# Performance work log

Hardware: AMD Instinct MI355X
Metric: run time of the kernel (lower is better)

The kernel has to match this reference:

```python
import jax, jax.numpy as jnp
import numpy as np

N = 32768      # num nodes
F = 128        # raw node feature dim
D = 128        # embedding_dim
E = 524288     # num edges (avg degree 16)
L = 8          # transformer depth
H = 8          # heads
CS = 32        # target_cluster_size
NC = 10        # num classes
K = N // CS    # num clusters (all full -> pad branch is a no-op)


def _leaky_relu(x):
    return jnp.where(x >= 0, x, 0.2 * x)


def _gat(h_in, src, dst, W, a_src, a_dst, b):
    # PyG GATConv, heads=1, with self-loops already appended to src/dst
    h = h_in @ W                                             # [N, D]
    e = _leaky_relu((h @ a_src)[src] + (h @ a_dst)[dst])     # [E+N]
    m = jax.ops.segment_max(e, dst, num_segments=N)
    ex = jnp.exp(e - m[dst])
    denom = jax.ops.segment_sum(ex, dst, num_segments=N)
    alpha = ex / denom[dst]
    return jax.ops.segment_sum(h[src] * alpha[:, None], dst, num_segments=N) + b


def _ln(x, s, b):
    m = x.mean(-1, keepdims=True)
    v = ((x - m) ** 2).mean(-1, keepdims=True)
    return (x - m) * jax.lax.rsqrt(v + 1e-5) * s + b


def setup_inputs() -> dict:
    key = jax.random.key(0)
    ks = jax.random.split(key, 20)
    rn = lambda k, s, sc=0.05: jax.random.normal(k, s, jnp.float32) * sc
    return dict(
        x=jax.random.normal(ks[0], (N, F), jnp.float32),
        edge_index=jax.random.randint(ks[1], (2, E), 0, N),
        node_order=jax.random.permutation(ks[2], N).astype(jnp.int32),
        W_in=rn(ks[3], (F, D)), b_in=jnp.zeros(D, jnp.float32),
        Wg1=rn(ks[4], (D, D)), as1=rn(ks[5], (D,)), ad1=rn(ks[6], (D,)), bg1=jnp.zeros(D, jnp.float32),
        Wg2=rn(ks[7], (D, D)), as2=rn(ks[8], (D,)), ad2=rn(ks[9], (D,)), bg2=jnp.zeros(D, jnp.float32),
        W_emb=rn(ks[10], (CS * D, D), 0.02), b_emb=jnp.zeros(D, jnp.float32),
        cls_tok=rn(ks[11], (D,)),
        ln1_s=jnp.ones((L, D), jnp.float32), ln1_b=jnp.zeros((L, D), jnp.float32),
        Wqkv=rn(ks[12], (L, D, 3 * D)), bqkv=jnp.zeros((L, 3 * D), jnp.float32),
        Wo=rn(ks[13], (L, D, D)), bo=jnp.zeros((L, D), jnp.float32),
        ln2_s=jnp.ones((L, D), jnp.float32), ln2_b=jnp.zeros((L, D), jnp.float32),
        Wf1=rn(ks[14], (L, D, 4 * D)), bf1=jnp.zeros((L, 4 * D), jnp.float32),
        Wf2=rn(ks[15], (L, 4 * D, D)), bf2=jnp.zeros((L, D), jnp.float32),
        Wc=rn(ks[16], (D, NC)), bc=jnp.zeros(NC, jnp.float32),
    )


def reference(x, edge_index, node_order, W_in, b_in, Wg1, as1, ad1, bg1,
              Wg2, as2, ad2, bg2, W_emb, b_emb, cls_tok,
              ln1_s, ln1_b, Wqkv, bqkv, Wo, bo, ln2_s, ln2_b,
              Wf1, bf1, Wf2, bf2, Wc, bc):
    loops = jnp.arange(N, dtype=edge_index.dtype)
    src = jnp.concatenate([edge_index[0], loops])
    dst = jnp.concatenate([edge_index[1], loops])
    h = x @ W_in + b_in
    h = _gat(h, src, dst, Wg1, as1, ad1, bg1)
    h = _gat(h, src, dst, Wg2, as2, ad2, bg2)
    # irregular cluster gather, then per-cluster linear embedding (32*D -> D)
    flat = h[node_order].reshape(K, CS * D)
    emb = flat @ W_emb + b_emb                               # [K, D]
    t = jnp.concatenate([cls_tok[None, :], emb], axis=0)     # [K+1, D]
    dh = D // H
    scale = dh ** -0.5
    for l in range(L):                                       # pre-norm transformer
        u = _ln(t, ln1_s[l], ln1_b[l])
        qkv = u @ Wqkv[l] + bqkv[l]
        q, k, v = [a.reshape(-1, H, dh) for a in jnp.split(qkv, 3, axis=-1)]
        att = jax.nn.softmax(jnp.einsum('qhd,khd->hqk', q, k) * scale, axis=-1)
        o = jnp.einsum('hqk,khd->qhd', att, v).reshape(-1, D) @ Wo[l] + bo[l]
        t = t + o
        u = _ln(t, ln2_s[l], ln2_b[l])
        t = t + jax.nn.gelu(u @ Wf1[l] + bf1[l]) @ Wf2[l] + bf2[l]
    return (t[0] @ Wc + bc)[None, :]                         # [1, NC]
```

## Files before the change

### kernel.cpp

```cpp
#include <hip/hip_runtime.h>
#include <hip/hip_bf16.h>
#include <math.h>

#define NN 32768
#define NE 524288
#define EN_TOT (NE + NN)
#define LL 8
#define SS 1025
#define SPLIT 16

__global__ void hist_kernel(const int* __restrict__ ei, int* __restrict__ cnt) {
    int i = blockIdx.x * 256 + threadIdx.x;
    if (i >= EN_TOT) return;
    int d = (i < NE) ? ei[NE + i] : (i - NE);
    atomicAdd(&cnt[d], 1);
}

__global__ void scan_kernel(const int* __restrict__ cnt, int* __restrict__ offs) {
    __shared__ int wsum[16];
    int t = threadIdx.x;
    int base = t * 32;
    int s = 0;
    #pragma unroll
    for (int j = 0; j < 32; ++j) s += cnt[base + j];
    int lane = t & 63, w = t >> 6;
    int v = s;
    #pragma unroll
    for (int d = 1; d < 64; d <<= 1) {
        int u = __shfl_up(v, d);
        if (lane >= d) v += u;
    }
    if (lane == 63) wsum[w] = v;
    __syncthreads();
    if (t == 0) {
        int a = 0;
        #pragma unroll
        for (int i = 0; i < 16; ++i) { int x = wsum[i]; wsum[i] = a; a += x; }
    }
    __syncthreads();
    int run = wsum[w] + (v - s);
    #pragma unroll
    for (int j = 0; j < 32; ++j) { offs[base + j] = run; run += cnt[base + j]; }
    if (t == 1023) offs[NN] = run;
}

__global__ void scatter_kernel(const int* __restrict__ ei, const int* __restrict__ offs,
                               int* __restrict__ fill, int* __restrict__ csr) {
    int i = blockIdx.x * 256 + threadIdx.x;
    if (i >= EN_TOT) return;
    int s, d;
    if (i < NE) { s = ei[i]; d = ei[NE + i]; } else { s = d = i - NE; }
    int pos = offs[d] + atomicAdd(&fill[d], 1);
    csr[pos] = s;
}

__device__ __forceinline__ float gelu_f(float x) {
    float x3 = x * x * x;
    return 0.5f * x * (1.f + tanhf(0.7978845608028654f * (x + 0.044715f * x3)));
}

__global__ void gemm_f32(const float* __restrict__ A, const float* __restrict__ B,
                         const float* __restrict__ bias, const float* res,
                         float* C, __hip_bfloat16* Cb,
                         const float* __restrict__ asv, const float* __restrict__ adv,
                         float* ssv, float* sdv,
                         int M, int Nn, int K) {
    __shared__ float As[32][66];
    __shared__ float Bs[32][72];
    int t = threadIdx.x;
    int bx = blockIdx.x, by = blockIdx.y;
    int tx = t & 15, ty = t >> 4;
    float acc[4][4] = {};
    int m0 = t >> 3;
    int kk4 = (t & 7) * 4;
    int kb0 = t >> 4;
    int n40 = (t & 15) * 4;

    for (int k0 = 0; k0 < K; k0 += 32) {
        __syncthreads();
        #pragma unroll
        for (int half = 0; half < 2; ++half) {
            int m = m0 + half * 32;
            int row = by * 64 + m;
            float4 v = {0.f, 0.f, 0.f, 0.f};
            if (row < M) v = *(const float4*)&A[(size_t)row * K + k0 + kk4];
            As[kk4 + 0][m] = v.x; As[kk4 + 1][m] = v.y;
            As[kk4 + 2][m] = v.z; As[kk4 + 3][m] = v.w;
        }
        #pragma unroll
        for (int half = 0; half < 2; ++half) {
            int kk = kb0 + half * 16;
            *(float4*)&Bs[kk][n40] = *(const float4*)&B[(size_t)(k0 + kk) * Nn + bx * 64 + n40];
        }
        __syncthreads();
        #pragma unroll
        for (int kk = 0; kk < 32; ++kk) {
            float a0 = As[kk][ty * 4 + 0];
            float a1 = As[kk][ty * 4 + 1];
            float a2 = As[kk][ty * 4 + 2];
            float a3 = As[kk][ty * 4 + 3];
            float4 b4 = *(float4*)&Bs[kk][tx * 4];
            acc[0][0] += a0 * b4.x; acc[0][1] += a0 * b4.y; acc[0][2] += a0 * b4.z; acc[0][3] += a0 * b4.w;
            acc[1][0] += a1 * b4.x; acc[1][1] += a1 * b4.y; acc[1][2] += a1 * b4.z; acc[1][3] += a1 * b4.w;
            acc[2][0] += a2 * b4.x; acc[2][1] += a2 * b4.y; acc[2][2] += a2 * b4.z; acc[2][3] += a2 * b4.w;
            acc[3][0] += a3 * b4.x; acc[3][1] += a3 * b4.y; acc[3][2] += a3 * b4.z; acc[3][3] += a3 * b4.w;
        }
    }
    #pragma unroll
    for (int i = 0; i < 4; ++i) {
        int row = by * 64 + ty * 4 + i;
        if (row < M) {
            #pragma unroll
            for (int j = 0; j < 4; ++j) {
                int col = bx * 64 + tx * 4 + j;
                float v = acc[i][j];
                if (bias) v += bias[col];
                if (res) v += res[(size_t)row * Nn + col];
                acc[i][j] = v;
                C[(size_t)row * Nn + col] = v;
                if (Cb) Cb[(size_t)row * Nn + col] = __float2bfloat16(v);
            }
        }
    }
    if (asv) {
        #pragma unroll
        for (int i = 0; i < 4; ++i) {
            int row = by * 64 + ty * 4 + i;
            float vs = 0.f, vd = 0.f;
            #pragma unroll
            for (int j = 0; j < 4; ++j) {
                int col = bx * 64 + tx * 4 + j;
                vs += acc[i][j] * asv[col];
                vd += acc[i][j] * adv[col];
            }
            #pragma unroll
            for (int m = 8; m >= 1; m >>= 1) { vs += __shfl_xor(vs, m); vd += __shfl_xor(vd, m); }
            if (tx == 0 && row < M) {
                atomicAdd(&ssv[row], vs);
                atomicAdd(&sdv[row], vd);
            }
        }
    }
}

__global__ void bcomb_kernel(const float* __restrict__ b_in, const float* __restrict__ Wg1,
                             float* __restrict__ bcomb) {
    int n = threadIdx.x;
    float s = 0.f;
    for (int k = 0; k < 128; ++k) s += b_in[k] * Wg1[k * 128 + n];
    bcomb[n] = s;
}

__global__ void emb_gemm(const float* __restrict__ h, const float* __restrict__ W,
                         const int* __restrict__ no, float* __restrict__ pbuf) {
    __shared__ float As[32][66];
    __shared__ float Bs[32][72];
    int t = threadIdx.x;
    int bx = blockIdx.x, by = blockIdx.y, sp = blockIdx.z;
    int tx = t & 15, ty = t >> 4;
    float acc[4][4] = {};
    int m0 = t >> 3;
    int kk4 = (t & 7) * 4;
    int kb0 = t >> 4;
    int n40 = (t & 15) * 4;
    int kbase = sp * 256;

    for (int k0 = 0; k0 < 256; k0 += 32) {
        __syncthreads();
        #pragma unroll
        for (int half = 0; half < 2; ++half) {
            int m = m0 + half * 32;
            int row = by * 64 + m;
            int kg = kbase + k0 + kk4;
            int node = no[row * 32 + (kg >> 7)];
            float4 v = *(const float4*)&h[(size_t)node * 128 + (kg & 127)];
            As[kk4 + 0][m] = v.x; As[kk4 + 1][m] = v.y;
            As[kk4 + 2][m] = v.z; As[kk4 + 3][m] = v.w;
        }
        #pragma unroll
        for (int half = 0; half < 2; ++half) {
            int kk = kb0 + half * 16;
            *(float4*)&Bs[kk][n40] = *(const float4*)&W[(size_t)(kbase + k0 + kk) * 128 + bx * 64 + n40];
        }
        __syncthreads();
        #pragma unroll
        for (int kk = 0; kk < 32; ++kk) {
            float a0 = As[kk][ty * 4 + 0];
            float a1 = As[kk][ty * 4 + 1];
            float a2 = As[kk][ty * 4 + 2];
            float a3 = As[kk][ty * 4 + 3];
            float4 b4 = *(float4*)&Bs[kk][tx * 4];
            acc[0][0] += a0 * b4.x; acc[0][1] += a0 * b4.y; acc[0][2] += a0 * b4.z; acc[0][3] += a0 * b4.w;
            acc[1][0] += a1 * b4.x; acc[1][1] += a1 * b4.y; acc[1][2] += a1 * b4.z; acc[1][3] += a1 * b4.w;
            acc[2][0] += a2 * b4.x; acc[2][1] += a2 * b4.y; acc[2][2] += a2 * b4.z; acc[2][3] += a2 * b4.w;
            acc[3][0] += a3 * b4.x; acc[3][1] += a3 * b4.y; acc[3][2] += a3 * b4.z; acc[3][3] += a3 * b4.w;
        }
    }
    float* C = pbuf + (size_t)sp * (1024 * 128);
    #pragma unroll
    for (int i = 0; i < 4; ++i) {
        int row = by * 64 + ty * 4 + i;
        #pragma unroll
        for (int j = 0; j < 4; ++j)
            C[(size_t)row * 128 + bx * 64 + tx * 4 + j] = acc[i][j];
    }
}

__global__ void emb_reduce(const float* __restrict__ pbuf, const float* __restrict__ b_emb,
                           float* __restrict__ out) {
    int i = blockIdx.x * 256 + threadIdx.x;
    float s = b_emb[i & 127];
    #pragma unroll
    for (int sp = 0; sp < SPLIT; ++sp) s += pbuf[(size_t)sp * 131072 + i];
    out[i] = s;
}

__global__ void gat_aggregate(const unsigned* __restrict__ hWb, const int* __restrict__ offs,
                              const int* __restrict__ csr, const float* __restrict__ ssrc,
                              const float* __restrict__ sdst, const float* __restrict__ bias,
                              float* __restrict__ out) {
    int lane = threadIdx.x & 63;
    int n = blockIdx.x * 4 + (threadIdx.x >> 6);
    int beg = offs[n], end = offs[n + 1];
    float sd = sdst[n];
    float mymax = -INFINITY;
    for (int p = beg + lane; p < end; p += 64) {
        float e = ssrc[csr[p]] + sd;
        e = (e >= 0.f) ? e : 0.2f * e;
        mymax = fmaxf(mymax, e);
    }
    #pragma unroll
    for (int m = 32; m >= 1; m >>= 1) mymax = fmaxf(mymax, __shfl_xor(mymax, m));
    float mysum = 0.f;
    for (int p = beg + lane; p < end; p += 64) {
        float e = ssrc[csr[p]] + sd;
        e = (e >= 0.f) ? e : 0.2f * e;
        mysum += __expf(e - mymax);
    }
    #pragma unroll
    for (int m = 32; m >= 1; m >>= 1) mysum += __shfl_xor(mysum, m);
    float inv = 1.f / mysum;
    float acc0 = 0.f, acc1 = 0.f;
    for (int p = beg; p < end; ++p) {
        int s = csr[p];
        float e = ssrc[s] + sd;
        e = (e >= 0.f) ? e : 0.2f * e;
        float al = __expf(e - mymax) * inv;
        unsigned u = hWb[(size_t)s * 64 + lane];
        float f0 = __uint_as_float(u << 16);
        float f1 = __uint_as_float(u & 0xffff0000u);
        acc0 += al * f0;
        acc1 += al * f1;
    }
    float2 ov;
    ov.x = acc0 + bias[2 * lane];
    ov.y = acc1 + bias[2 * lane + 1];
    *(float2*)&out[(size_t)n * 128 + 2 * lane] = ov;
}

__global__ __launch_bounds__(256) void qkv_slice(
        const float* __restrict__ tb, const float* __restrict__ s1, const float* __restrict__ b1,
        const float* __restrict__ Wq, const float* __restrict__ bq, float* __restrict__ qkv) {
    __shared__ float u[4][128];
    __shared__ float red[4][2][128];
    __shared__ float ws[8192];
    int t = threadIdx.x;
    int r0 = blockIdx.x * 4, sl = blockIdx.y;
    int col = t & 127, kh = t >> 7;
    {
        int rw = t >> 6, lane = t & 63;
        int row = r0 + rw;
        float a0 = 0.f, a1 = 0.f;
        if (row < SS) {
            a0 = tb[(size_t)row * 128 + lane];
            a1 = tb[(size_t)row * 128 + 64 + lane];
        }
        float sm = a0 + a1;
        #pragma unroll
        for (int m = 32; m >= 1; m >>= 1) sm += __shfl_xor(sm, m);
        float mean = sm * (1.f / 128.f);
        float d0 = a0 - mean, d1 = a1 - mean;
        float vv = d0 * d0 + d1 * d1;
        #pragma unroll
        for (int m = 32; m >= 1; m >>= 1) vv += __shfl_xor(vv, m);
        float rs = rsqrtf(vv * (1.f / 128.f) + 1e-5f);
        u[rw][lane] = d0 * rs * s1[lane] + b1[lane];
        u[rw][64 + lane] = d1 * rs * s1[64 + lane] + b1[64 + lane];
    }
    float acc[4] = {};
    for (int k0 = 0; k0 < 128; k0 += 64) {
        __syncthreads();
        const float* src = Wq + (size_t)k0 * 384 + sl * 128;
        #pragma unroll
        for (int i = 0; i < 8; ++i) {
            int idx = i * 256 + t;
            int kk = idx >> 5, c4 = (idx & 31) * 4;
            ((float4*)ws)[idx] = *(const float4*)&src[(size_t)kk * 384 + c4];
        }
        __syncthreads();
        int kb = kh * 32;
        #pragma unroll
        for (int kq = 0; kq < 32; kq += 4) {
            float a4[4][4];
            #pragma unroll
            for (int i = 0; i < 4; ++i)
                *(float4*)a4[i] = *(const float4*)&u[i][k0 + kb + kq];
            #pragma unroll
            for (int q = 0; q < 4; ++q) {
                float b = ws[(kb + kq + q) * 128 + col];
                #pragma unroll
                for (int i = 0; i < 4; ++i) acc[i] += a4[i][q] * b;
            }
        }
    }
    __syncthreads();
    #pragma unroll
    for (int i = 0; i < 4; ++i) red[i][kh][col] = acc[i];
    __syncthreads();
    if (t < 128) {
        float bqv = bq[sl * 128 + t];
        #pragma unroll
        for (int i = 0; i < 4; ++i) {
            int row = r0 + i;
            if (row < SS)
                qkv[(size_t)row * 384 + sl * 128 + t] = red[i][0][t] + red[i][1][t] + bqv;
        }
    }
}

__global__ __launch_bounds__(256) void proj_ln2(
        const float* __restrict__ ao, const float* __restrict__ Wo, const float* __restrict__ bo,
        const float* __restrict__ s2, const float* __restrict__ b2, const float* __restrict__ bf2,
        float* __restrict__ tb, float* __restrict__ ub) {
    __shared__ float bufA[4][128];
    __shared__ float tn[4][128];
    __shared__ float red[4][2][128];
    __shared__ float ws[8192];
    int t = threadIdx.x;
    int r0 = blockIdx.x * 4;
    int lane = t & 63;
    int col = t & 127, kh = t >> 7;
    {
        int rw = t >> 6;
        int row = r0 + rw;
        float a0 = 0.f, a1 = 0.f;
        if (row < SS) {
            a0 = ao[(size_t)row * 128 + lane];
            a1 = ao[(size_t)row * 128 + 64 + lane];
        }
        bufA[rw][lane] = a0;
        bufA[rw][64 + lane] = a1;
    }
    float pp[4] = {};
    for (int k0 = 0; k0 < 128; k0 += 64) {
        __syncthreads();
        const float4* src = (const float4*)&Wo[(size_t)k0 * 128];
        #pragma unroll
        for (int i = 0; i < 8; ++i) ((float4*)ws)[i * 256 + t] = src[i * 256 + t];
        __syncthreads();
        int kb = kh * 32;
        #pragma unroll
        for (int kq = 0; kq < 32; kq += 4) {
            float a4[4][4];
            #pragma unroll
            for (int i = 0; i < 4; ++i)
                *(float4*)a4[i] = *(const float4*)&bufA[i][k0 + kb + kq];
            #pragma unroll
            for (int q = 0; q < 4; ++q) {
                float b = ws[(kb + kq + q) * 128 + col];
                #pragma unroll
                for (int i = 0; i < 4; ++i) pp[i] += a4[i][q] * b;
            }
        }
    }
    __syncthreads();
    #pragma unroll
    for (int i = 0; i < 4; ++i) red[i][kh][col] = pp[i];
    __syncthreads();
    if (t < 128) {
        #pragma unroll
        for (int i = 0; i < 4; ++i) {
            int row = r0 + i;
            float v = 0.f;
            if (row < SS) {
                v = red[i][0][t] + red[i][1][t] + bo[t] + tb[(size_t)row * 128 + t];
                tb[(size_t)row * 128 + t] = v + bf2[t];
            }
            tn[i][t] = v;
        }
    }
    __syncthreads();
    {
        int rw = t >> 6;
        int row = r0 + rw;
        float a0 = tn[rw][lane], a1 = tn[rw][64 + lane];
        float sm = a0 + a1;
        #pragma unroll
        for (int m = 32; m >= 1; m >>= 1) sm += __shfl_xor(sm, m);
        float mean = sm * (1.f / 128.f);
        float d0 = a0 - mean, d1 = a1 - mean;
        float vv = d0 * d0 + d1 * d1;
        #pragma unroll
        for (int m = 32; m >= 1; m >>= 1) vv += __shfl_xor(vv, m);
        float rs = rsqrtf(vv * (1.f / 128.f) + 1e-5f);
        if (row < SS) {
            ub[(size_t)row * 128 + lane] = d0 * rs * s2[lane] + b2[lane];
            ub[(size_t)row * 128 + 64 + lane] = d1 * rs * s2[64 + lane] + b2[64 + lane];
        }
    }
}

__global__ __launch_bounds__(256) void ffn_part(
        const float* __restrict__ ub, const float* __restrict__ Wf1, const float* __restrict__ bf1,
        const float* __restrict__ Wf2, float* __restrict__ tb) {
    __shared__ float u[4][128];
    __shared__ float g[4][128];
    __shared__ float red[4][2][128];
    __shared__ float ws[8192];
    int t = threadIdx.x;
    int r0 = blockIdx.x * 4, sl = blockIdx.y;
    int col = t & 127, kh = t >> 7;
    {
        int rw = t >> 6, lane = t & 63;
        int row = r0 + rw;
        float a0 = 0.f, a1 = 0.f;
        if (row < SS) {
            a0 = ub[(size_t)row * 128 + lane];
            a1 = ub[(size_t)row * 128 + 64 + lane];
        }
        u[rw][lane] = a0;
        u[rw][64 + lane] = a1;
    }
    float a1c[4] = {};
    for (int k0 = 0; k0 < 128; k0 += 64) {
        __syncthreads();
        const float* src = Wf1 + (size_t)k0 * 512 + sl * 128;
        #pragma unroll
        for (int i = 0; i < 8; ++i) {
            int idx = i * 256 + t;
            int kk = idx >> 5, c4 = (idx & 31) * 4;
            ((float4*)ws)[idx] = *(const float4*)&src[(size_t)kk * 512 + c4];
        }
        __syncthreads();
        int kb = kh * 32;
        #pragma unroll
        for (int kq = 0; kq < 32; kq += 4) {
            float a4[4][4];
            #pragma unroll
            for (int i = 0; i < 4; ++i)
                *(float4*)a4[i] = *(const float4*)&u[i][k0 + kb + kq];
            #pragma unroll
            for (int q = 0; q < 4; ++q) {
                float b = ws[(kb + kq + q) * 128 + col];
                #pragma unroll
                for (int i = 0; i < 4; ++i) a1c[i] += a4[i][q] * b;
            }
        }
    }
    __syncthreads();
    #pragma unroll
    for (int i = 0; i < 4; ++i) red[i][kh][col] = a1c[i];
    __syncthreads();
    if (t < 128) {
        float bv = bf1[sl * 128 + t];
        #pragma unroll
        for (int i = 0; i < 4; ++i)
            g[i][t] = gelu_f(red[i][0][t] + red[i][1][t] + bv);
    }
    float a2c[4] = {};
    for (int k0 = 0; k0 < 128; k0 += 64) {
        __syncthreads();
        const float4* src = (const float4*)&Wf2[(size_t)(sl * 128 + k0) * 128];
        #pragma unroll
        for (int i = 0; i < 8; ++i) ((float4*)ws)[i * 256 + t] = src[i * 256 + t];
        __syncthreads();
        int kb = kh * 32;
        #pragma unroll
        for (int kq = 0; kq < 32; kq += 4) {
            float a4[4][4];
            #pragma unroll
            for (int i = 0; i < 4; ++i)
                *(float4*)a4[i] = *(const float4*)&g[i][k0 + kb + kq];
            #pragma unroll
            for (int q = 0; q < 4; ++q) {
                float b = ws[(kb + kq + q) * 128 + col];
                #pragma unroll
                for (int i = 0; i < 4; ++i) a2c[i] += a4[i][q] * b;
            }
        }
    }
    __syncthreads();
    #pragma unroll
    for (int i = 0; i < 4; ++i) red[i][kh][col] = a2c[i];
    __syncthreads();
    if (t < 128) {
        #pragma unroll
        for (int i = 0; i < 4; ++i) {
            int row = r0 + i;
            if (row < SS)
                atomicAdd(&tb[(size_t)row * 128 + t], red[i][0][t] + red[i][1][t]);
        }
    }
}

__global__ void attn_kernel(const float* __restrict__ qkv, float* __restrict__ ao) {
    __shared__ float Kl[64][20];
    __shared__ float Vl[64][20];
    int h = blockIdx.y;
    int t = threadIdx.x;
    int sub = t & 15;
    int qr = blockIdx.x * 16 + (t >> 4);
    bool active = qr < SS;
    float q[16];
    if (active) {
        #pragma unroll
        for (int d = 0; d < 16; ++d) q[d] = qkv[(size_t)qr * 384 + h * 16 + d];
    }
    float m = -INFINITY, sum = 0.f;
    float acc[16] = {};
    for (int j0 = 0; j0 < SS; j0 += 64) {
        __syncthreads();
        int j = t >> 2, dg = (t & 3) * 4;
        if (j0 + j < SS) {
            const float* row = qkv + (size_t)(j0 + j) * 384 + h * 16 + dg;
            *(float4*)&Kl[j][dg] = *(const float4*)(row + 128);
            *(float4*)&Vl[j][dg] = *(const float4*)(row + 256);
        }
        __syncthreads();
        if (active) {
            int jmax = min(64, SS - j0);
            for (int jj = sub; jj < jmax; jj += 16) {
                float4 ka = *(const float4*)&Kl[jj][0];
                float4 kb = *(const float4*)&Kl[jj][4];
                float4 kc = *(const float4*)&Kl[jj][8];
                float4 kd = *(const float4*)&Kl[jj][12];
                float sc = q[0]*ka.x + q[1]*ka.y + q[2]*ka.z + q[3]*ka.w
                         + q[4]*kb.x + q[5]*kb.y + q[6]*kb.z + q[7]*kb.w
                         + q[8]*kc.x + q[9]*kc.y + q[10]*kc.z + q[11]*kc.w
                         + q[12]*kd.x + q[13]*kd.y + q[14]*kd.z + q[15]*kd.w;
                sc *= 0.25f;
                float4 va = *(const float4*)&Vl[jj][0];
                float4 vb = *(const float4*)&Vl[jj][4];
                float4 vc = *(const float4*)&Vl[jj][8];
                float4 vd = *(const float4*)&Vl[jj][12];
                float vv[16] = {va.x, va.y, va.z, va.w, vb.x, vb.y, vb.z, vb.w,
                                vc.x, vc.y, vc.z, vc.w, vd.x, vd.y, vd.z, vd.w};
                if (sc <= m) {
                    float p = __expf(sc - m);
                    sum += p;
                    #pragma unroll
                    for (int d = 0; d < 16; ++d) acc[d] += p * vv[d];
                } else {
                    float c = __expf(m - sc);
                    sum = sum * c + 1.f;
                    #pragma unroll
                    for (int d = 0; d < 16; ++d) acc[d] = acc[d] * c + vv[d];
                    m = sc;
                }
            }
        }
    }
    if (active) {
        #pragma unroll
        for (int msk = 1; msk < 16; msk <<= 1) {
            float mo = __shfl_xor(m, msk);
            float so = __shfl_xor(sum, msk);
            float vo[16];
            #pragma unroll
            for (int d = 0; d < 16; ++d) vo[d] = __shfl_xor(acc[d], msk);
            float mn = fmaxf(m, mo);
            float c1 = __expf(m - mn), c2 = __expf(mo - mn);
            sum = sum * c1 + so * c2;
            #pragma unroll
            for (int d = 0; d < 16; ++d) acc[d] = acc[d] * c1 + vo[d] * c2;
            m = mn;
        }
        if (sub == 0) {
            float inv = 1.f / sum;
            #pragma unroll
            for (int d = 0; d < 16; ++d) ao[(size_t)qr * 128 + h * 16 + d] = acc[d] * inv;
        }
    }
}

__global__ void cls_copy(const float* __restrict__ c, float* __restrict__ t) {
    t[threadIdx.x] = c[threadIdx.x];
}

__global__ void classifier_kernel(const float* __restrict__ t, const float* __restrict__ Wc,
                                  const float* __restrict__ bc, float* __restrict__ out) {
    int j = threadIdx.x;
    if (j < 10) {
        float a = bc[j];
        #pragma unroll
        for (int k = 0; k < 128; ++k) a += t[k] * Wc[k * 10 + j];
        out[j] = a;
    }
}

extern "C" void kernel_launch(void* const* d_in, const int* in_sizes, int n_in,
                              void* d_out, int out_size, void* d_ws, size_t ws_size,
                              hipStream_t stream) {
    (void)in_sizes; (void)n_in; (void)out_size; (void)ws_size;
    const float* x     = (const float*)d_in[0];
    const int*   ei    = (const int*)d_in[1];
    const int*   nord  = (const int*)d_in[2];
    const float* W_in  = (const float*)d_in[3];
    const float* b_in  = (const float*)d_in[4];
    const float* Wg1   = (const float*)d_in[5];
    const float* as1   = (const float*)d_in[6];
    const float* ad1   = (const float*)d_in[7];
    const float* bg1   = (const float*)d_in[8];
    const float* Wg2   = (const float*)d_in[9];
    const float* as2   = (const float*)d_in[10];
    const float* ad2   = (const float*)d_in[11];
    const float* bg2   = (const float*)d_in[12];
    const float* W_emb = (const float*)d_in[13];
    const float* b_emb = (const float*)d_in[14];
    const float* clst  = (const float*)d_in[15];
    const float* ln1s  = (const float*)d_in[16];
    const float* ln1b  = (const float*)d_in[17];
    const float* Wqkv  = (const float*)d_in[18];
    const float* bqkv  = (const float*)d_in[19];
    const float* Wo    = (const float*)d_in[20];
    const float* bo    = (const float*)d_in[21];
    const float* ln2s  = (const float*)d_in[22];
    const float* ln2b  = (const float*)d_in[23];
    const float* Wf1   = (const float*)d_in[24];
    const float* bf1   = (const float*)d_in[25];
    const float* Wf2   = (const float*)d_in[26];
    const float* bf2   = (const float*)d_in[27];
    const float* Wc    = (const float*)d_in[28];
    const float* bc    = (const float*)d_in[29];

    char* w = (char*)d_ws;
    size_t o = 0;
    auto ALLOC = [&](size_t nbytes) -> char* {
        char* p = w + o;
        o += (nbytes + 255) & ~(size_t)255;
        return p;
    };
    int*   cnt   = (int*)ALLOC((size_t)NN * 4);
    int*   fill  = (int*)ALLOC((size_t)NN * 4);
    int*   offs  = (int*)ALLOC((size_t)(NN + 1) * 4);
    int*   csr   = (int*)ALLOC((size_t)EN_TOT * 4);
    float* hA    = (float*)ALLOC((size_t)NN * 128 * 4);
    float* hW    = (float*)ALLOC((size_t)NN * 128 * 4);
    float* h1    = (float*)ALLOC((size_t)NN * 128 * 4);
    __hip_bfloat16* hWb = (__hip_bfloat16*)ALLOC((size_t)NN * 128 * 2);
    float* ssrc  = (float*)ALLOC((size_t)NN * 4);
    float* sdst  = (float*)ALLOC((size_t)NN * 4);
    float* tbuf  = (float*)ALLOC((size_t)SS * 128 * 4);
    float* ubuf  = (float*)ALLOC((size_t)SS * 128 * 4);
    float* qkvb  = (float*)ALLOC((size_t)SS * 384 * 4);
    float* aob   = (float*)ALLOC((size_t)SS * 128 * 4);
    float* Wcomb = (float*)ALLOC((size_t)128 * 128 * 4);
    float* bcomb = (float*)ALLOC((size_t)128 * 4);
    float* pbuf  = hW;

    dim3 blk(256);
    int egrid = (EN_TOT + 255) / 256;

    hipMemsetAsync(cnt, 0, (size_t)NN * 8, stream);
    hist_kernel<<<egrid, blk, 0, stream>>>(ei, cnt);
    scan_kernel<<<1, 1024, 0, stream>>>(cnt, offs);
    scatter_kernel<<<egrid, blk, 0, stream>>>(ei, offs, fill, csr);

    gemm_f32<<<dim3(2, 2), blk, 0, stream>>>(W_in, Wg1, nullptr, nullptr, Wcomb,
                                             nullptr, nullptr, nullptr, nullptr, nullptr,
                                             128, 128, 128);
    bcomb_kernel<<<1, 128, 0, stream>>>(b_in, Wg1, bcomb);

    hipMemsetAsync(ssrc, 0, (size_t)NN * 8, stream);
    gemm_f32<<<dim3(2, 512), blk, 0, stream>>>(x, Wcomb, bcomb, nullptr, hW,
                                               hWb, as1, ad1, ssrc, sdst,
                                               NN, 128, 128);
    gat_aggregate<<<8192, blk, 0, stream>>>((const unsigned*)hWb, offs, csr, ssrc, sdst, bg1, h1);
    hipMemsetAsync(ssrc, 0, (size_t)NN * 8, stream);
    gemm_f32<<<dim3(2, 512), blk, 0, stream>>>(h1, Wg2, nullptr, nullptr, hW,
                                               hWb, as2, ad2, ssrc, sdst,
                                               NN, 128, 128);
    gat_aggregate<<<8192, blk, 0, stream>>>((const unsigned*)hWb, offs, csr, ssrc, sdst, bg2, hA);

    cls_copy<<<1, 128, 0, stream>>>(clst, tbuf);
    emb_gemm<<<dim3(2, 16, SPLIT), blk, 0, stream>>>(hA, W_emb, nord, pbuf);
    emb_reduce<<<512, blk, 0, stream>>>(pbuf, b_emb, tbuf + 128);

    for (int l = 0; l < LL; ++l) {
        qkv_slice<<<dim3(257, 3), blk, 0, stream>>>(tbuf, ln1s + l * 128, ln1b + l * 128,
                                                    Wqkv + (size_t)l * 128 * 384, bqkv + l * 384, qkvb);
        attn_kernel<<<dim3(65, 8), blk, 0, stream>>>(qkvb, aob);
        proj_ln2<<<257, blk, 0, stream>>>(aob, Wo + (size_t)l * 128 * 128, bo + l * 128,
                                          ln2s + l * 128, ln2b + l * 128, bf2 + l * 128,
                                          tbuf, ubuf);
        ffn_part<<<dim3(257, 4), blk, 0, stream>>>(ubuf, Wf1 + (size_t)l * 128 * 512, bf1 + l * 512,
                                                   Wf2 + (size_t)l * 512 * 128, tbuf);
    }
    classifier_kernel<<<1, 64, 0, stream>>>(tbuf, Wc, bc, (float*)d_out);
}
```

Baseline: 874.2 us.

## Split GAT dots out, gather fp32 rows, pre-gather cluster input, deterministic FFN partials

The GEMM epilogue no longer computes the attention logit dots with atomics or emits a bf16 copy. A separate dots kernel computes them per node, and aggregation now reads fp32 features with lane-parallel edge loading and shuffle broadcast. The cluster gather is materialized into a flat buffer before the embedding GEMM. FFN slices write per-slice partial buffers that are summed on read, replacing atomics, and the attention K/V tile grows to 128. This trades extra launches and doubled gather bandwidth (fp32 instead of bf16) for fewer atomics and more memory-level parallelism in the edge loop.

```diff
diff --git a/kernel.cpp b/kernel.cpp
--- a/kernel.cpp
+++ b/kernel.cpp
@@ -8,6 +8,7 @@
 #define LL 8
 #define SS 1025
 #define SPLIT 16
+#define SS128 (SS * 128)
 
 __global__ void hist_kernel(const int* __restrict__ ei, int* __restrict__ cnt) {
     int i = blockIdx.x * 256 + threadIdx.x;
@@ -61,10 +62,7 @@
 
 __global__ void gemm_f32(const float* __restrict__ A, const float* __restrict__ B,
                          const float* __restrict__ bias, const float* res,
-                         float* C, __hip_bfloat16* Cb,
-                         const float* __restrict__ asv, const float* __restrict__ adv,
-                         float* ssv, float* sdv,
-                         int M, int Nn, int K) {
+                         float* C, int M, int Nn, int K) {
     __shared__ float As[32][66];
     __shared__ float Bs[32][72];
     int t = threadIdx.x;
@@ -116,28 +114,7 @@
                 float v = acc[i][j];
                 if (bias) v += bias[col];
                 if (res) v += res[(size_t)row * Nn + col];
-                acc[i][j] = v;
                 C[(size_t)row * Nn + col] = v;
-                if (Cb) Cb[(size_t)row * Nn + col] = __float2bfloat16(v);
-            }
-        }
-    }
-    if (asv) {
-        #pragma unroll
-        for (int i = 0; i < 4; ++i) {
-            int row = by * 64 + ty * 4 + i;
-            float vs = 0.f, vd = 0.f;
-            #pragma unroll
-            for (int j = 0; j < 4; ++j) {
-                int col = bx * 64 + tx * 4 + j;
-                vs += acc[i][j] * asv[col];
-                vd += acc[i][j] * adv[col];
-            }
-            #pragma unroll
-            for (int m = 8; m >= 1; m >>= 1) { vs += __shfl_xor(vs, m); vd += __shfl_xor(vd, m); }
-            if (tx == 0 && row < M) {
-                atomicAdd(&ssv[row], vs);
-                atomicAdd(&sdv[row], vd);
             }
         }
     }
@@ -151,71 +128,21 @@
     bcomb[n] = s;
 }
 
-__global__ void emb_gemm(const float* __restrict__ h, const float* __restrict__ W,
-                         const int* __restrict__ no, float* __restrict__ pbuf) {
-    __shared__ float As[32][66];
-    __shared__ float Bs[32][72];
-    int t = threadIdx.x;
-    int bx = blockIdx.x, by = blockIdx.y, sp = blockIdx.z;
-    int tx = t & 15, ty = t >> 4;
-    float acc[4][4] = {};
-    int m0 = t >> 3;
-    int kk4 = (t & 7) * 4;
-    int kb0 = t >> 4;
-    int n40 = (t & 15) * 4;
-    int kbase = sp * 256;
-
-    for (int k0 = 0; k0 < 256; k0 += 32) {
-        __syncthreads();
-        #pragma unroll
-        for (int half = 0; half < 2; ++half) {
-            int m = m0 + half * 32;
-            int row = by * 64 + m;
-            int kg = kbase + k0 + kk4;
-            int node = no[row * 32 + (kg >> 7)];
-            float4 v = *(const float4*)&h[(size_t)node * 128 + (kg & 127)];
-            As[kk4 + 0][m] = v.x; As[kk4 + 1][m] = v.y;
-            As[kk4 + 2][m] = v.z; As[kk4 + 3][m] = v.w;
-        }
-        #pragma unroll
-        for (int half = 0; half < 2; ++half) {
-            int kk = kb0 + half * 16;
-            *(float4*)&Bs[kk][n40] = *(const float4*)&W[(size_t)(kbase + k0 + kk) * 128 + bx * 64 + n40];
-        }
-        __syncthreads();
-        #pragma unroll
-        for (int kk = 0; kk < 32; ++kk) {
-            float a0 = As[kk][ty * 4 + 0];
-            float a1 = As[kk][ty * 4 + 1];
-            float a2 = As[kk][ty * 4 + 2];
-            float a3 = As[kk][ty * 4 + 3];
-            float4 b4 = *(float4*)&Bs[kk][tx * 4];
-            acc[0][0] += a0 * b4.x; acc[0][1] += a0 * b4.y; acc[0][2] += a0 * b4.z; acc[0][3] += a0 * b4.w;
-            acc[1][0] += a1 * b4.x; acc[1][1] += a1 * b4.y; acc[1][2] += a1 * b4.z; acc[1][3] += a1 * b4.w;
-            acc[2][0] += a2 * b4.x; acc[2][1] += a2 * b4.y; acc[2][2] += a2 * b4.z; acc[2][3] += a2 * b4.w;
-            acc[3][0] += a3 * b4.x; acc[3][1] += a3 * b4.y; acc[3][2] += a3 * b4.z; acc[3][3] += a3 * b4.w;
-        }
-    }
-    float* C = pbuf + (size_t)sp * (1024 * 128);
-    #pragma unroll
-    for (int i = 0; i < 4; ++i) {
-        int row = by * 64 + ty * 4 + i;
-        #pragma unroll
-        for (int j = 0; j < 4; ++j)
-            C[(size_t)row * 128 + bx * 64 + tx * 4 + j] = acc[i][j];
-    }
-}
-
-__global__ void emb_reduce(const float* __restrict__ pbuf, const float* __restrict__ b_emb,
-                           float* __restrict__ out) {
-    int i = blockIdx.x * 256 + threadIdx.x;
-    float s = b_emb[i & 127];
-    #pragma unroll
-    for (int sp = 0; sp < SPLIT; ++sp) s += pbuf[(size_t)sp * 131072 + i];
-    out[i] = s;
-}
-
-__global__ void gat_aggregate(const unsigned* __restrict__ hWb, const int* __restrict__ offs,
+__global__ void dots_kernel(const float* __restrict__ hW, const float* __restrict__ asrc,
+                            const float* __restrict__ adst, float* __restrict__ ss,
+                            float* __restrict__ sd) {
+    int lane = threadIdx.x & 63;
+    int n = blockIdx.x * 4 + (threadIdx.x >> 6);
+    float h0 = hW[(size_t)n * 128 + lane];
+    float h1 = hW[(size_t)n * 128 + 64 + lane];
+    float vs = h0 * asrc[lane] + h1 * asrc[64 + lane];
+    float vd = h0 * adst[lane] + h1 * adst[64 + lane];
+    #pragma unroll
+    for (int m = 32; m >= 1; m >>= 1) { vs += __shfl_xor(vs, m); vd += __shfl_xor(vd, m); }
+    if (lane == 0) { ss[n] = vs; sd[n] = vd; }
+}
+
+__global__ void gat_aggregate(const float* __restrict__ hW, const int* __restrict__ offs,
                               const int* __restrict__ csr, const float* __restrict__ ssrc,
                               const float* __restrict__ sdst, const float* __restrict__ bias,
                               float* __restrict__ out) {
@@ -240,26 +167,124 @@
     #pragma unroll
     for (int m = 32; m >= 1; m >>= 1) mysum += __shfl_xor(mysum, m);
     float inv = 1.f / mysum;
-    float acc0 = 0.f, acc1 = 0.f;
-    for (int p = beg; p < end; ++p) {
-        int s = csr[p];
-        float e = ssrc[s] + sd;
-        e = (e >= 0.f) ? e : 0.2f * e;
-        float al = __expf(e - mymax) * inv;
-        unsigned u = hWb[(size_t)s * 64 + lane];
-        float f0 = __uint_as_float(u << 16);
-        float f1 = __uint_as_float(u & 0xffff0000u);
-        acc0 += al * f0;
-        acc1 += al * f1;
+    float accx = 0.f, accy = 0.f;
+    int deg = end - beg;
+    for (int c0 = 0; c0 < deg; c0 += 64) {
+        int s = 0; float al = 0.f;
+        if (c0 + lane < deg) {
+            s = csr[beg + c0 + lane];
+            float e = ssrc[s] + sd;
+            e = (e >= 0.f) ? e : 0.2f * e;
+            al = __expf(e - mymax) * inv;
+        }
+        int cend = min(64, deg - c0);
+        int p = 0;
+        for (; p + 4 <= cend; p += 4) {
+            int s0 = __shfl(s, p);     float a0 = __shfl(al, p);
+            int s1 = __shfl(s, p + 1); float a1 = __shfl(al, p + 1);
+            int s2 = __shfl(s, p + 2); float a2 = __shfl(al, p + 2);
+            int s3 = __shfl(s, p + 3); float a3 = __shfl(al, p + 3);
+            float2 v0 = *(const float2*)&hW[(size_t)s0 * 128 + lane * 2];
+            float2 v1 = *(const float2*)&hW[(size_t)s1 * 128 + lane * 2];
+            float2 v2 = *(const float2*)&hW[(size_t)s2 * 128 + lane * 2];
+            float2 v3 = *(const float2*)&hW[(size_t)s3 * 128 + lane * 2];
+            accx += a0 * v0.x; accy += a0 * v0.y;
+            accx += a1 * v1.x; accy += a1 * v1.y;
+            accx += a2 * v2.x; accy += a2 * v2.y;
+            accx += a3 * v3.x; accy += a3 * v3.y;
+        }
+        for (; p < cend; ++p) {
+            int sj = __shfl(s, p);
+            float aj = __shfl(al, p);
+            float2 v = *(const float2*)&hW[(size_t)sj * 128 + lane * 2];
+            accx += aj * v.x; accy += aj * v.y;
+        }
     }
     float2 ov;
-    ov.x = acc0 + bias[2 * lane];
-    ov.y = acc1 + bias[2 * lane + 1];
+    ov.x = accx + bias[2 * lane];
+    ov.y = accy + bias[2 * lane + 1];
     *(float2*)&out[(size_t)n * 128 + 2 * lane] = ov;
 }
 
+__global__ void gather_copy(const float* __restrict__ hA, const int* __restrict__ no,
+                            float* __restrict__ flat) {
+    int i = blockIdx.x * 256 + threadIdx.x;
+    int m = i >> 12, j = i & 4095;
+    int node = no[(m << 5) + (j >> 7)];
+    flat[i] = hA[(size_t)node * 128 + (j & 127)];
+}
+
+__global__ void emb_gemm(const float* __restrict__ flat, const float* __restrict__ W,
+                         float* __restrict__ pbuf) {
+    __shared__ float As[32][66];
+    __shared__ float Bs[32][72];
+    int t = threadIdx.x;
+    int bx = blockIdx.x, by = blockIdx.y, sp = blockIdx.z;
+    int tx = t & 15, ty = t >> 4;
+    float acc[4][4] = {};
+    int m0 = t >> 3;
+    int kk4 = (t & 7) * 4;
+    int kb0 = t >> 4;
+    int n40 = (t & 15) * 4;
+    int kbase = sp * 256;
+
+    for (int k0 = 0; k0 < 256; k0 += 32) {
+        __syncthreads();
+        #pragma unroll
+        for (int half = 0; half < 2; ++half) {
+            int m = m0 + half * 32;
+            int row = by * 64 + m;
+            float4 v = *(const float4*)&flat[(size_t)row * 4096 + kbase + k0 + kk4];
+            As[kk4 + 0][m] = v.x; As[kk4 + 1][m] = v.y;
+            As[kk4 + 2][m] = v.z; As[kk4 + 3][m] = v.w;
+        }
+        #pragma unroll
+        for (int half = 0; half < 2; ++half) {
+            int kk = kb0 + half * 16;
+            *(float4*)&Bs[kk][n40] = *(const float4*)&W[(size_t)(kbase + k0 + kk) * 128 + bx * 64 + n40];
+        }
+        __syncthreads();
+        #pragma unroll
+        for (int kk = 0; kk < 32; ++kk) {
+            float a0 = As[kk][ty * 4 + 0];
+            float a1 = As[kk][ty * 4 + 1];
+            float a2 = As[kk][ty * 4 + 2];
+            float a3 = As[kk][ty * 4 + 3];
+            float4 b4 = *(float4*)&Bs[kk][tx * 4];
+            acc[0][0] += a0 * b4.x; acc[0][1] += a0 * b4.y; acc[0][2] += a0 * b4.z; acc[0][3] += a0 * b4.w;
+            acc[1][0] += a1 * b4.x; acc[1][1] += a1 * b4.y; acc[1][2] += a1 * b4.z; acc[1][3] += a1 * b4.w;
+            acc[2][0] += a2 * b4.x; acc[2][1] += a2 * b4.y; acc[2][2] += a2 * b4.z; acc[2][3] += a2 * b4.w;
+            acc[3][0] += a3 * b4.x; acc[3][1] += a3 * b4.y; acc[3][2] += a3 * b4.z; acc[3][3] += a3 * b4.w;
+        }
+    }
+    float* C = pbuf + (size_t)sp * (1024 * 128);
+    #pragma unroll
+    for (int i = 0; i < 4; ++i) {
+        int row = by * 64 + ty * 4 + i;
+        #pragma unroll
+        for (int j = 0; j < 4; ++j)
+            C[(size_t)row * 128 + bx * 64 + tx * 4 + j] = acc[i][j];
+    }
+}
+
+__global__ void emb_reduce(const float* __restrict__ pbuf, const float* __restrict__ b_emb,
+                           const float* __restrict__ cls, float* __restrict__ tb) {
+    int i = blockIdx.x * 256 + threadIdx.x;
+    if (blockIdx.x == 0 && threadIdx.x < 128) tb[threadIdx.x] = cls[threadIdx.x];
+    float s = b_emb[i & 127];
+    #pragma unroll
+    for (int sp = 0; sp < SPLIT; ++sp) s += pbuf[(size_t)sp * 131072 + i];
+    tb[128 + i] = s;
+}
+
+__device__ __forceinline__ float tok_read(const float* __restrict__ tb, const float* __restrict__ P,
+                                          size_t ix) {
+    return tb[ix] + P[ix] + P[SS128 + ix] + P[2 * (size_t)SS128 + ix] + P[3 * (size_t)SS128 + ix];
+}
+
 __global__ __launch_bounds__(256) void qkv_slice(
-        const float* __restrict__ tb, const float* __restrict__ s1, const float* __restrict__ b1,
+        const float* __restrict__ tb, const float* __restrict__ P,
+        const float* __restrict__ s1, const float* __restrict__ b1,
         const float* __restrict__ Wq, const float* __restrict__ bq, float* __restrict__ qkv) {
     __shared__ float u[4][128];
     __shared__ float red[4][2][128];
@@ -272,8 +297,9 @@
         int row = r0 + rw;
         float a0 = 0.f, a1 = 0.f;
         if (row < SS) {
-            a0 = tb[(size_t)row * 128 + lane];
-            a1 = tb[(size_t)row * 128 + 64 + lane];
+            size_t ix = (size_t)row * 128 + lane;
+            a0 = tok_read(tb, P, ix);
+            a1 = tok_read(tb, P, ix + 64);
         }
         float sm = a0 + a1;
         #pragma unroll
@@ -329,7 +355,8 @@
 }
 
 __global__ __launch_bounds__(256) void proj_ln2(
-        const float* __restrict__ ao, const float* __restrict__ Wo, const float* __restrict__ bo,
+        const float* __restrict__ ao, const float* __restrict__ P,
+        const float* __restrict__ Wo, const float* __restrict__ bo,
         const float* __restrict__ s2, const float* __restrict__ b2, const float* __restrict__ bf2,
         float* __restrict__ tb, float* __restrict__ ub) {
     __shared__ float bufA[4][128];
@@ -383,8 +410,10 @@
             int row = r0 + i;
             float v = 0.f;
             if (row < SS) {
-                v = red[i][0][t] + red[i][1][t] + bo[t] + tb[(size_t)row * 128 + t];
-                tb[(size_t)row * 128 + t] = v + bf2[t];
+                size_t ix = (size_t)row * 128 + t;
+                float told = tok_read(tb, P, ix);
+                v = red[i][0][t] + red[i][1][t] + bo[t] + told;
+                tb[ix] = v + bf2[t];
             }
             tn[i][t] = v;
         }
@@ -412,7 +441,7 @@
 
 __global__ __launch_bounds__(256) void ffn_part(
         const float* __restrict__ ub, const float* __restrict__ Wf1, const float* __restrict__ bf1,
-        const float* __restrict__ Wf2, float* __restrict__ tb) {
+        const float* __restrict__ Wf2, float* __restrict__ P) {
     __shared__ float u[4][128];
     __shared__ float g[4][128];
     __shared__ float red[4][2][128];
@@ -498,14 +527,14 @@
         for (int i = 0; i < 4; ++i) {
             int row = r0 + i;
             if (row < SS)
-                atomicAdd(&tb[(size_t)row * 128 + t], red[i][0][t] + red[i][1][t]);
+                P[(size_t)sl * SS128 + (size_t)row * 128 + t] = red[i][0][t] + red[i][1][t];
         }
     }
 }
 
 __global__ void attn_kernel(const float* __restrict__ qkv, float* __restrict__ ao) {
-    __shared__ float Kl[64][20];
-    __shared__ float Vl[64][20];
+    __shared__ float Kl[128][20];
+    __shared__ float Vl[128][20];
     int h = blockIdx.y;
     int t = threadIdx.x;
     int sub = t & 15;
@@ -518,17 +547,19 @@
     }
     float m = -INFINITY, sum = 0.f;
     float acc[16] = {};
-    for (int j0 = 0; j0 < SS; j0 += 64) {
-        __syncthreads();
-        int j = t >> 2, dg = (t & 3) * 4;
+    for (int j0 = 0; j0 < SS; j0 += 128) {
+        __syncthreads();
+        int j = t >> 1, dg = (t & 1) * 8;
         if (j0 + j < SS) {
             const float* row = qkv + (size_t)(j0 + j) * 384 + h * 16 + dg;
-            *(float4*)&Kl[j][dg] = *(const float4*)(row + 128);
-            *(float4*)&Vl[j][dg] = *(const float4*)(row + 256);
+            *(float4*)&Kl[j][dg]     = *(const float4*)(row + 128);
+            *(float4*)&Kl[j][dg + 4] = *(const float4*)(row + 132);
+            *(float4*)&Vl[j][dg]     = *(const float4*)(row + 256);
+            *(float4*)&Vl[j][dg + 4] = *(const float4*)(row + 260);
         }
         __syncthreads();
         if (active) {
-            int jmax = min(64, SS - j0);
+            int jmax = min(128, SS - j0);
             for (int jj = sub; jj < jmax; jj += 16) {
                 float4 ka = *(const float4*)&Kl[jj][0];
                 float4 kb = *(const float4*)&Kl[jj][4];
@@ -583,17 +614,14 @@
     }
 }
 
-__global__ void cls_copy(const float* __restrict__ c, float* __restrict__ t) {
-    t[threadIdx.x] = c[threadIdx.x];
-}
-
-__global__ void classifier_kernel(const float* __restrict__ t, const float* __restrict__ Wc,
-                                  const float* __restrict__ bc, float* __restrict__ out) {
+__global__ void classifier_kernel(const float* __restrict__ tb, const float* __restrict__ P,
+                                  const float* __restrict__ Wc, const float* __restrict__ bc,
+                                  float* __restrict__ out) {
     int j = threadIdx.x;
     if (j < 10) {
         float a = bc[j];
         #pragma unroll
-        for (int k = 0; k < 128; ++k) a += t[k] * Wc[k * 10 + j];
+        for (int k = 0; k < 128; ++k) a += tok_read(tb, P, k) * Wc[k * 10 + j];
         out[j] = a;
     }
 }
@@ -647,16 +675,17 @@
     float* hA    = (float*)ALLOC((size_t)NN * 128 * 4);
     float* hW    = (float*)ALLOC((size_t)NN * 128 * 4);
     float* h1    = (float*)ALLOC((size_t)NN * 128 * 4);
-    __hip_bfloat16* hWb = (__hip_bfloat16*)ALLOC((size_t)NN * 128 * 2);
     float* ssrc  = (float*)ALLOC((size_t)NN * 4);
     float* sdst  = (float*)ALLOC((size_t)NN * 4);
-    float* tbuf  = (float*)ALLOC((size_t)SS * 128 * 4);
-    float* ubuf  = (float*)ALLOC((size_t)SS * 128 * 4);
+    float* tbuf  = (float*)ALLOC((size_t)SS128 * 4);
+    float* ubuf  = (float*)ALLOC((size_t)SS128 * 4);
     float* qkvb  = (float*)ALLOC((size_t)SS * 384 * 4);
-    float* aob   = (float*)ALLOC((size_t)SS * 128 * 4);
+    float* aob   = (float*)ALLOC((size_t)SS128 * 4);
+    float* Pbuf  = (float*)ALLOC((size_t)4 * SS128 * 4);
     float* Wcomb = (float*)ALLOC((size_t)128 * 128 * 4);
     float* bcomb = (float*)ALLOC((size_t)128 * 4);
     float* pbuf  = hW;
+    float* flat  = h1;
 
     dim3 blk(256);
     int egrid = (EN_TOT + 255) / 256;
@@ -666,35 +695,31 @@
     scan_kernel<<<1, 1024, 0, stream>>>(cnt, offs);
     scatter_kernel<<<egrid, blk, 0, stream>>>(ei, offs, fill, csr);
 
-    gemm_f32<<<dim3(2, 2), blk, 0, stream>>>(W_in, Wg1, nullptr, nullptr, Wcomb,
-                                             nullptr, nullptr, nullptr, nullptr, nullptr,
-                                             128, 128, 128);
+    gemm_f32<<<dim3(2, 2), blk, 0, stream>>>(W_in, Wg1, nullptr, nullptr, Wcomb, 128, 128, 128);
     bcomb_kernel<<<1, 128, 0, stream>>>(b_in, Wg1, bcomb);
 
-    hipMemsetAsync(ssrc, 0, (size_t)NN * 8, stream);
-    gemm_f32<<<dim3(2, 512), blk, 0, stream>>>(x, Wcomb, bcomb, nullptr, hW,
-                                               hWb, as1, ad1, ssrc, sdst,
-                                               NN, 128, 128);
-    gat_aggregate<<<8192, blk, 0, stream>>>((const unsigned*)hWb, offs, csr, ssrc, sdst, bg1, h1);
-    hipMemsetAsync(ssrc, 0, (size_t)NN * 8, stream);
-    gemm_f32<<<dim3(2, 512), blk, 0, stream>>>(h1, Wg2, nullptr, nullptr, hW,
-                                               hWb, as2, ad2, ssrc, sdst,
-                                               NN, 128, 128);
-    gat_aggregate<<<8192, blk, 0, stream>>>((const unsigned*)hWb, offs, csr, ssrc, sdst, bg2, hA);
-
-    cls_copy<<<1, 128, 0, stream>>>(clst, tbuf);
-    emb_gemm<<<dim3(2, 16, SPLIT), blk, 0, stream>>>(hA, W_emb, nord, pbuf);
-    emb_reduce<<<512, blk, 0, stream>>>(pbuf, b_emb, tbuf + 128);
+    gemm_f32<<<dim3(2, 512), blk, 0, stream>>>(x, Wcomb, bcomb, nullptr, hW, NN, 128, 128);
+    dots_kernel<<<8192, blk, 0, stream>>>(hW, as1, ad1, ssrc, sdst);
+    gat_aggregate<<<8192, blk, 0, stream>>>(hW, offs, csr, ssrc, sdst, bg1, h1);
+    gemm_f32<<<dim3(2, 512), blk, 0, stream>>>(h1, Wg2, nullptr, nullptr, hW, NN, 128, 128);
+    dots_kernel<<<8192, blk, 0, stream>>>(hW, as2, ad2, ssrc, sdst);
+    gat_aggregate<<<8192, blk, 0, stream>>>(hW, offs, csr, ssrc, sdst, bg2, hA);
+
+    gather_copy<<<16384, blk, 0, stream>>>(hA, nord, flat);
+    emb_gemm<<<dim3(2, 16, SPLIT), blk, 0, stream>>>(flat, W_emb, pbuf);
+    emb_reduce<<<512, blk, 0, stream>>>(pbuf, b_emb, clst, tbuf);
+
+    hipMemsetAsync(Pbuf, 0, (size_t)4 * SS128 * 4, stream);
 
     for (int l = 0; l < LL; ++l) {
-        qkv_slice<<<dim3(257, 3), blk, 0, stream>>>(tbuf, ln1s + l * 128, ln1b + l * 128,
+        qkv_slice<<<dim3(257, 3), blk, 0, stream>>>(tbuf, Pbuf, ln1s + l * 128, ln1b + l * 128,
                                                     Wqkv + (size_t)l * 128 * 384, bqkv + l * 384, qkvb);
         attn_kernel<<<dim3(65, 8), blk, 0, stream>>>(qkvb, aob);
-        proj_ln2<<<257, blk, 0, stream>>>(aob, Wo + (size_t)l * 128 * 128, bo + l * 128,
+        proj_ln2<<<257, blk, 0, stream>>>(aob, Pbuf, Wo + (size_t)l * 128 * 128, bo + l * 128,
                                           ln2s + l * 128, ln2b + l * 128, bf2 + l * 128,
                                           tbuf, ubuf);
         ffn_part<<<dim3(257, 4), blk, 0, stream>>>(ubuf, Wf1 + (size_t)l * 128 * 512, bf1 + l * 512,
-                                                   Wf2 + (size_t)l * 512 * 128, tbuf);
-    }
-    classifier_kernel<<<1, 64, 0, stream>>>(tbuf, Wc, bc, (float*)d_out);
-}
+                                                   Wf2 + (size_t)l * 512 * 128, Pbuf);
+    }
+    classifier_kernel<<<1, 64, 0, stream>>>(tbuf, Pbuf, Wc, bc, (float*)d_out);
+}
```

Result: faster. 851.8 us (-2.6%).
